# Performance work log

Hardware: AMD Instinct MI355X
Metric: run time of the kernel (lower is better)

The kernel has to match this reference:

```python
import jax, jax.numpy as jnp
import numpy as np

DT = 0.05
TAU = 10.0
V_TH = 2.0
ALPHA = 1.0 - DT / TAU  # membrane leak factor (1 - dt/tau)


def setup_inputs() -> dict:
    key = jax.random.key(0)
    kx, kw = jax.random.split(key)
    B, T, N = 32, 1024, 2048
    x = jax.random.normal(kx, (B, T, N), dtype=jnp.float32)
    # w ~ Normal(0, 1/sqrt(N)) as in torch.nn.init.normal_(std=1/sqrt(N))
    w = jax.random.normal(kw, (N,), dtype=jnp.float32) * float(1.0 / np.sqrt(N))
    return {"x": x, "w": w}


def reference(x, w):
    """LIF recurrence with online eligibility-trace gradient, fused over time.

    Per step t (matching NeuronClass.__call__ then backward_online):
      v   = alpha*v + x_t @ w - v_th * z          (z from previous step, detached)
      z   = 1[v > v_th]
      eps = x_t - v * w                            # [B, N]
      g  += v * eps + (eps @ w) * p                # p is the PRE-update trace
      p   = alpha*p + x_t
    Returns (v_seq [B,T], z_seq [B,T], grad_acc [B,N]).
    """
    B, T, N = x.shape
    alpha = jnp.asarray(ALPHA, x.dtype)
    v_th = jnp.asarray(V_TH, x.dtype)
    xt = jnp.swapaxes(x, 0, 1)  # [T, B, N] for scan over time

    def step(carry, x_t):
        v, z, p, g = carry
        v = alpha * v + x_t @ w - v_th * z          # [B]
        z = (v > v_th).astype(x_t.dtype)            # hard threshold
        eps = x_t - v[:, None] * w                  # [B, N] prediction error
        g = g + v[:, None] * eps + (eps @ w)[:, None] * p
        p = alpha * p + x_t                         # trace updated AFTER use
        return (v, z, p, g), (v, z)

    v0 = jnp.zeros((B,), x.dtype)
    z0 = jnp.zeros((B,), x.dtype)
    p0 = jnp.zeros((B, N), x.dtype)
    g0 = jnp.zeros((B, N), x.dtype)
    (_, _, _, grad_acc), (v_seq, z_seq) = jax.lax.scan(step, (v0, z0, p0, g0), xt)
    return jnp.swapaxes(v_seq, 0, 1), jnp.swapaxes(z_seq, 0, 1), grad_acc
```

## Files before the change

### kernel.cpp

```cpp
#include <hip/hip_runtime.h>


#define ALPHA 0.995f
#define VTH   2.0f

constexpr int B = 32;
constexpr int T = 1024;
constexpr int N = 2048;
constexpr int CT  = 256;
constexpr int NCH = T / CT;
constexpr int TCH = 128;
constexpr int NTC = T / TCH;

typedef float floatx4 __attribute__((ext_vector_type(4)));

__device__ inline floatx4 ntload4(const float* p) {
    return __builtin_nontemporal_load(reinterpret_cast<const floatx4*>(p));
}

__global__ __launch_bounds__(256) void gemv_kernel(const float* __restrict__ x,
                                                   const float* __restrict__ w,
                                                   float* __restrict__ uT) {
    const int wave = threadIdx.x >> 6;
    const int lane = threadIdx.x & 63;
    const int row0 = blockIdx.x * 16 + wave * 4;
    const float* xr = x + (size_t)row0 * N;
    float s0 = 0.f, s1 = 0.f, s2 = 0.f, s3 = 0.f;
#pragma unroll
    for (int k = 0; k < 8; ++k) {
        const int idx = k * 256 + lane * 4;
        const floatx4 wv = *reinterpret_cast<const floatx4*>(w + idx);
        const floatx4 a = ntload4(xr + idx);
        const floatx4 b = ntload4(xr + N + idx);
        const floatx4 c = ntload4(xr + 2 * N + idx);
        const floatx4 d = ntload4(xr + 3 * N + idx);
        s0 += a.x * wv.x + a.y * wv.y + a.z * wv.z + a.w * wv.w;
        s1 += b.x * wv.x + b.y * wv.y + b.z * wv.z + b.w * wv.w;
        s2 += c.x * wv.x + c.y * wv.y + c.z * wv.z + c.w * wv.w;
        s3 += d.x * wv.x + d.y * wv.y + d.z * wv.z + d.w * wv.w;
    }
#pragma unroll
    for (int off = 32; off; off >>= 1) {
        s0 += __shfl_down(s0, off);
        s1 += __shfl_down(s1, off);
        s2 += __shfl_down(s2, off);
        s3 += __shfl_down(s3, off);
    }
    if (lane == 0) {
        const int b0 = row0 >> 10;
        const int t0 = row0 & 1023;
        uT[(t0 + 0) * B + b0] = s0;
        uT[(t0 + 1) * B + b0] = s1;
        uT[(t0 + 2) * B + b0] = s2;
        uT[(t0 + 3) * B + b0] = s3;
    }
}

__global__ __launch_bounds__(256) void scan_kernel(const float* __restrict__ w,
                                                   const float* __restrict__ ubuf,
                                                   float* __restrict__ sbuf,
                                                   float* __restrict__ cbuf,
                                                   float* __restrict__ V2,
                                                   float* __restrict__ out_v,
                                                   float* __restrict__ out_z) {
    __shared__ float u_lds[CT * B];
    __shared__ float v_st[CT * B];
    const int tid  = threadIdx.x;
    const int lane = tid & 63;

    float wacc = 0.f;
#pragma unroll
    for (int i = 0; i < N / 64; ++i) {
        const float wv = w[i * 64 + lane];
        wacc += wv * wv;
    }
#pragma unroll
    for (int off = 32; off; off >>= 1) wacc += __shfl_xor(wacc, off);
    const float wsq = wacc;

    float v = 0.f, z = 0.f, v2 = 0.f;

    for (int cc = 0; cc < NCH; ++cc) {
        const int base = cc * CT * B;
        const int t0   = cc * CT;
#pragma unroll
        for (int k = 0; k < 8; ++k) {
            const int j = k * 1024 + tid * 4;
            *reinterpret_cast<floatx4*>(&u_lds[j]) =
                *reinterpret_cast<const floatx4*>(&ubuf[base + j]);
        }
        __syncthreads();
        if (tid < 32) {
            const int b = tid;
#pragma unroll 4
            for (int tt = 0; tt < CT; ++tt) {
                const float ut = u_lds[tt * 32 + b];
                v = ALPHA * v + ut - VTH * z;
                z = (v > VTH) ? 1.f : 0.f;
                u_lds[tt * 32 + b] = ut - v * wsq;
                v_st[tt * 32 + ((b + tt) & 31)] = v;
                v2 += v * v;
            }
        }
        __syncthreads();
#pragma unroll
        for (int k = 0; k < 8; ++k) {
            const int j = k * 1024 + tid * 4;
            *reinterpret_cast<floatx4*>(&sbuf[base + j]) =
                *reinterpret_cast<const floatx4*>(&u_lds[j]);
        }
#pragma unroll
        for (int k = 0; k < 32; ++k) {
            const int idx = k * 256 + tid;
            const int b  = idx >> 8;
            const int tt = idx & 255;
            const float vv = v_st[tt * 32 + ((b + tt) & 31)];
            out_v[b * T + t0 + tt] = vv;
            out_z[b * T + t0 + tt] = (vv > VTH) ? 1.f : 0.f;
        }
        __syncthreads();
    }
    if (tid < 32) V2[tid] = v2;

    float q = 0.f;
    for (int cc = NCH - 1; cc >= 0; --cc) {
        const int base = cc * CT * B;
        const int t0   = cc * CT;
#pragma unroll
        for (int k = 0; k < 8; ++k) {
            const int j = k * 1024 + tid * 4;
            *reinterpret_cast<floatx4*>(&u_lds[j]) =
                *reinterpret_cast<const floatx4*>(&sbuf[base + j]);
        }
#pragma unroll
        for (int k = 0; k < 32; ++k) {
            const int idx = k * 256 + tid;
            const int b  = idx >> 8;
            const int tt = idx & 255;
            v_st[tt * 32 + ((b + tt) & 31)] = out_v[b * T + t0 + tt];
        }
        __syncthreads();
        if (tid < 32) {
            const int b = tid;
#pragma unroll 4
            for (int tt = CT - 1; tt >= 0; --tt) {
                const float st = u_lds[tt * 32 + b];
                const float vt = v_st[tt * 32 + ((b + tt) & 31)];
                u_lds[tt * 32 + b] = vt + q;
                q = st + ALPHA * q;
            }
        }
        __syncthreads();
#pragma unroll
        for (int k = 0; k < 8; ++k) {
            const int j = k * 1024 + tid * 4;
            *reinterpret_cast<floatx4*>(&cbuf[base + j]) =
                *reinterpret_cast<const floatx4*>(&u_lds[j]);
        }
        __syncthreads();
    }
}

__global__ __launch_bounds__(256) void accum_kernel(const float* __restrict__ x,
                                                    const float* __restrict__ cT,
                                                    float* __restrict__ gpart) {
    __shared__ float cs[TCH];
    const int b   = blockIdx.z;
    const int nc  = blockIdx.y;
    const int tc  = blockIdx.x;
    const int t0  = tc * TCH;
    const int tid = threadIdx.x;
    if (tid < TCH) cs[tid] = cT[(t0 + tid) * B + b];
    __syncthreads();

    const int n = nc * 1024 + tid * 4;
    const float* xb = x + ((size_t)b * T + t0) * N + n;
    floatx4 acc = {0.f, 0.f, 0.f, 0.f};
#pragma unroll 4
    for (int tt = 0; tt < TCH; ++tt) {
        const floatx4 xv = ntload4(xb + (size_t)tt * N);
        const float c = cs[tt];
        acc.x += c * xv.x;
        acc.y += c * xv.y;
        acc.z += c * xv.z;
        acc.w += c * xv.w;
    }
    *reinterpret_cast<floatx4*>(gpart + ((size_t)tc * B + b) * N + n) = acc;
}

__global__ __launch_bounds__(256) void reduce_kernel(const float* __restrict__ gpart,
                                                     const float* __restrict__ w,
                                                     const float* __restrict__ V2,
                                                     float* __restrict__ g) {
    const int i = blockIdx.x * 256 + threadIdx.x;
    const int b = i >> 11;
    const int n = i & (N - 1);
    float acc = -V2[b] * w[n];
#pragma unroll
    for (int tc = 0; tc < NTC; ++tc) acc += gpart[tc * (B * N) + i];
    g[i] = acc;
}

extern "C" void kernel_launch(void* const* d_in, const int* in_sizes, int n_in,
                              void* d_out, int out_size, void* d_ws, size_t ws_size,
                              hipStream_t stream) {
    const float* x = (const float*)d_in[0];
    const float* w = (const float*)d_in[1];

    float* out   = (float*)d_out;
    float* out_v = out;
    float* out_z = out + B * T;
    float* out_g = out + 2 * B * T;

    float* ubuf  = (float*)d_ws;
    float* sbuf  = ubuf + B * T;
    float* cbuf  = sbuf + B * T;
    float* V2    = cbuf + B * T;
    float* gpart = V2 + B;

    gemv_kernel<<<(B * T) / 16, 256, 0, stream>>>(x, w, ubuf);
    scan_kernel<<<1, 256, 0, stream>>>(w, ubuf, sbuf, cbuf, V2, out_v, out_z);
    accum_kernel<<<dim3(NTC, N / 1024, B), 256, 0, stream>>>(x, cbuf, gpart);
    reduce_kernel<<<(B * N) / 256, 256, 0, stream>>>(gpart, w, V2, out_g);
}
```

Measured before the change: 461.9 us.

## Split scan across one block per batch row with batch-major layout

The single-block scan kernel, which handled all 32 batch rows in chunked LDS passes, is replaced by 32 blocks of one wave each. In each block one lane runs the forward and backward recurrences over all timesteps held in LDS, using vectorized register blocks of 32 steps. The gemv output and the c buffer switch from time-major to batch-major layout, which removes the transposed stores and the global sbuf round trip. The accum loop unroll also rises from 4 to 8. The serial chain per row is still done by one lane, but rows now run in parallel on separate CUs and chunk synchronisation is gone.

```diff
diff --git a/kernel.cpp b/kernel.cpp
--- a/kernel.cpp
+++ b/kernel.cpp
@@ -7,8 +7,6 @@
 constexpr int B = 32;
 constexpr int T = 1024;
 constexpr int N = 2048;
-constexpr int CT  = 256;
-constexpr int NCH = T / CT;
 constexpr int TCH = 128;
 constexpr int NTC = T / TCH;
 
@@ -20,7 +18,7 @@
 
 __global__ __launch_bounds__(256) void gemv_kernel(const float* __restrict__ x,
                                                    const float* __restrict__ w,
-                                                   float* __restrict__ uT) {
+                                                   float* __restrict__ u) {
     const int wave = threadIdx.x >> 6;
     const int lane = threadIdx.x & 63;
     const int row0 = blockIdx.x * 16 + wave * 4;
@@ -47,26 +45,23 @@
         s3 += __shfl_down(s3, off);
     }
     if (lane == 0) {
-        const int b0 = row0 >> 10;
-        const int t0 = row0 & 1023;
-        uT[(t0 + 0) * B + b0] = s0;
-        uT[(t0 + 1) * B + b0] = s1;
-        uT[(t0 + 2) * B + b0] = s2;
-        uT[(t0 + 3) * B + b0] = s3;
-    }
-}
-
-__global__ __launch_bounds__(256) void scan_kernel(const float* __restrict__ w,
-                                                   const float* __restrict__ ubuf,
-                                                   float* __restrict__ sbuf,
-                                                   float* __restrict__ cbuf,
-                                                   float* __restrict__ V2,
-                                                   float* __restrict__ out_v,
-                                                   float* __restrict__ out_z) {
-    __shared__ float u_lds[CT * B];
-    __shared__ float v_st[CT * B];
-    const int tid  = threadIdx.x;
-    const int lane = tid & 63;
+        floatx4 r = {s0, s1, s2, s3};
+        *reinterpret_cast<floatx4*>(u + row0) = r;
+    }
+}
+
+__global__ __launch_bounds__(64) void scan_kernel(const float* __restrict__ w,
+                                                  const float* __restrict__ u,
+                                                  float* __restrict__ cbuf,
+                                                  float* __restrict__ V2,
+                                                  float* __restrict__ out_v,
+                                                  float* __restrict__ out_z) {
+    __shared__ float u_lds[T];
+    __shared__ float v_lds[T];
+    __shared__ float s_lds[T];
+    __shared__ float c_lds[T];
+    const int b    = blockIdx.x;
+    const int lane = threadIdx.x;
 
     float wacc = 0.f;
 #pragma unroll
@@ -78,91 +73,84 @@
     for (int off = 32; off; off >>= 1) wacc += __shfl_xor(wacc, off);
     const float wsq = wacc;
 
-    float v = 0.f, z = 0.f, v2 = 0.f;
-
-    for (int cc = 0; cc < NCH; ++cc) {
-        const int base = cc * CT * B;
-        const int t0   = cc * CT;
-#pragma unroll
-        for (int k = 0; k < 8; ++k) {
-            const int j = k * 1024 + tid * 4;
-            *reinterpret_cast<floatx4*>(&u_lds[j]) =
-                *reinterpret_cast<const floatx4*>(&ubuf[base + j]);
+#pragma unroll
+    for (int k = 0; k < T / 256; ++k) {
+        const int j = (k * 64 + lane) * 4;
+        *reinterpret_cast<floatx4*>(&u_lds[j]) =
+            *reinterpret_cast<const floatx4*>(&u[b * T + j]);
+    }
+    __syncthreads();
+
+    if (lane == 0) {
+        float v = 0.f, z = 0.f, v2 = 0.f;
+        for (int cc = 0; cc < T / 32; ++cc) {
+            const int base = cc * 32;
+            floatx4 ub[8];
+#pragma unroll
+            for (int k = 0; k < 8; ++k)
+                ub[k] = *reinterpret_cast<floatx4*>(&u_lds[base + k * 4]);
+            floatx4 vb[8], sb[8];
+#pragma unroll
+            for (int k = 0; k < 8; ++k) {
+#pragma unroll
+                for (int e = 0; e < 4; ++e) {
+                    const float ut = ub[k][e];
+                    v = ALPHA * v + ut - VTH * z;
+                    z = (v > VTH) ? 1.f : 0.f;
+                    vb[k][e] = v;
+                    sb[k][e] = ut - v * wsq;
+                    v2 += v * v;
+                }
+            }
+#pragma unroll
+            for (int k = 0; k < 8; ++k) {
+                *reinterpret_cast<floatx4*>(&v_lds[base + k * 4]) = vb[k];
+                *reinterpret_cast<floatx4*>(&s_lds[base + k * 4]) = sb[k];
+            }
         }
-        __syncthreads();
-        if (tid < 32) {
-            const int b = tid;
-#pragma unroll 4
-            for (int tt = 0; tt < CT; ++tt) {
-                const float ut = u_lds[tt * 32 + b];
-                v = ALPHA * v + ut - VTH * z;
-                z = (v > VTH) ? 1.f : 0.f;
-                u_lds[tt * 32 + b] = ut - v * wsq;
-                v_st[tt * 32 + ((b + tt) & 31)] = v;
-                v2 += v * v;
-            }
+        V2[b] = v2;
+        float q = 0.f;
+        for (int cc = T / 32 - 1; cc >= 0; --cc) {
+            const int base = cc * 32;
+            floatx4 sb[8], vb[8], cb[8];
+#pragma unroll
+            for (int k = 0; k < 8; ++k) {
+                sb[k] = *reinterpret_cast<floatx4*>(&s_lds[base + k * 4]);
+                vb[k] = *reinterpret_cast<floatx4*>(&v_lds[base + k * 4]);
+            }
+#pragma unroll
+            for (int k = 7; k >= 0; --k) {
+#pragma unroll
+                for (int e = 3; e >= 0; --e) {
+                    cb[k][e] = vb[k][e] + q;
+                    q = sb[k][e] + ALPHA * q;
+                }
+            }
+#pragma unroll
+            for (int k = 0; k < 8; ++k)
+                *reinterpret_cast<floatx4*>(&c_lds[base + k * 4]) = cb[k];
         }
-        __syncthreads();
-#pragma unroll
-        for (int k = 0; k < 8; ++k) {
-            const int j = k * 1024 + tid * 4;
-            *reinterpret_cast<floatx4*>(&sbuf[base + j]) =
-                *reinterpret_cast<const floatx4*>(&u_lds[j]);
-        }
-#pragma unroll
-        for (int k = 0; k < 32; ++k) {
-            const int idx = k * 256 + tid;
-            const int b  = idx >> 8;
-            const int tt = idx & 255;
-            const float vv = v_st[tt * 32 + ((b + tt) & 31)];
-            out_v[b * T + t0 + tt] = vv;
-            out_z[b * T + t0 + tt] = (vv > VTH) ? 1.f : 0.f;
-        }
-        __syncthreads();
-    }
-    if (tid < 32) V2[tid] = v2;
-
-    float q = 0.f;
-    for (int cc = NCH - 1; cc >= 0; --cc) {
-        const int base = cc * CT * B;
-        const int t0   = cc * CT;
-#pragma unroll
-        for (int k = 0; k < 8; ++k) {
-            const int j = k * 1024 + tid * 4;
-            *reinterpret_cast<floatx4*>(&u_lds[j]) =
-                *reinterpret_cast<const floatx4*>(&sbuf[base + j]);
-        }
-#pragma unroll
-        for (int k = 0; k < 32; ++k) {
-            const int idx = k * 256 + tid;
-            const int b  = idx >> 8;
-            const int tt = idx & 255;
-            v_st[tt * 32 + ((b + tt) & 31)] = out_v[b * T + t0 + tt];
-        }
-        __syncthreads();
-        if (tid < 32) {
-            const int b = tid;
-#pragma unroll 4
-            for (int tt = CT - 1; tt >= 0; --tt) {
-                const float st = u_lds[tt * 32 + b];
-                const float vt = v_st[tt * 32 + ((b + tt) & 31)];
-                u_lds[tt * 32 + b] = vt + q;
-                q = st + ALPHA * q;
-            }
-        }
-        __syncthreads();
-#pragma unroll
-        for (int k = 0; k < 8; ++k) {
-            const int j = k * 1024 + tid * 4;
-            *reinterpret_cast<floatx4*>(&cbuf[base + j]) =
-                *reinterpret_cast<const floatx4*>(&u_lds[j]);
-        }
-        __syncthreads();
+    }
+    __syncthreads();
+
+#pragma unroll
+    for (int k = 0; k < T / 256; ++k) {
+        const int j = (k * 64 + lane) * 4;
+        const floatx4 vv = *reinterpret_cast<floatx4*>(&v_lds[j]);
+        floatx4 zz;
+        zz.x = (vv.x > VTH) ? 1.f : 0.f;
+        zz.y = (vv.y > VTH) ? 1.f : 0.f;
+        zz.z = (vv.z > VTH) ? 1.f : 0.f;
+        zz.w = (vv.w > VTH) ? 1.f : 0.f;
+        *reinterpret_cast<floatx4*>(&out_v[b * T + j]) = vv;
+        *reinterpret_cast<floatx4*>(&out_z[b * T + j]) = zz;
+        *reinterpret_cast<floatx4*>(&cbuf[b * T + j]) =
+            *reinterpret_cast<floatx4*>(&c_lds[j]);
     }
 }
 
 __global__ __launch_bounds__(256) void accum_kernel(const float* __restrict__ x,
-                                                    const float* __restrict__ cT,
+                                                    const float* __restrict__ c,
                                                     float* __restrict__ gpart) {
     __shared__ float cs[TCH];
     const int b   = blockIdx.z;
@@ -170,20 +158,20 @@
     const int tc  = blockIdx.x;
     const int t0  = tc * TCH;
     const int tid = threadIdx.x;
-    if (tid < TCH) cs[tid] = cT[(t0 + tid) * B + b];
+    if (tid < TCH) cs[tid] = c[b * T + t0 + tid];
     __syncthreads();
 
     const int n = nc * 1024 + tid * 4;
     const float* xb = x + ((size_t)b * T + t0) * N + n;
     floatx4 acc = {0.f, 0.f, 0.f, 0.f};
-#pragma unroll 4
+#pragma unroll 8
     for (int tt = 0; tt < TCH; ++tt) {
         const floatx4 xv = ntload4(xb + (size_t)tt * N);
-        const float c = cs[tt];
-        acc.x += c * xv.x;
-        acc.y += c * xv.y;
-        acc.z += c * xv.z;
-        acc.w += c * xv.w;
+        const float cc = cs[tt];
+        acc.x += cc * xv.x;
+        acc.y += cc * xv.y;
+        acc.z += cc * xv.z;
+        acc.w += cc * xv.w;
     }
     *reinterpret_cast<floatx4*>(gpart + ((size_t)tc * B + b) * N + n) = acc;
 }
@@ -212,14 +200,13 @@
     float* out_z = out + B * T;
     float* out_g = out + 2 * B * T;
 
-    float* ubuf  = (float*)d_ws;
-    float* sbuf  = ubuf + B * T;
-    float* cbuf  = sbuf + B * T;
-    float* V2    = cbuf + B * T;
+    float* u     = (float*)d_ws;
+    float* c     = u + B * T;
+    float* V2    = c + B * T;
     float* gpart = V2 + B;
 
-    gemv_kernel<<<(B * T) / 16, 256, 0, stream>>>(x, w, ubuf);
-    scan_kernel<<<1, 256, 0, stream>>>(w, ubuf, sbuf, cbuf, V2, out_v, out_z);
-    accum_kernel<<<dim3(NTC, N / 1024, B), 256, 0, stream>>>(x, cbuf, gpart);
+    gemv_kernel<<<(B * T) / 16, 256, 0, stream>>>(x, w, u);
+    scan_kernel<<<B, 64, 0, stream>>>(w, u, c, V2, out_v, out_z);
+    accum_kernel<<<dim3(NTC, N / 1024, B), 256, 0, stream>>>(x, c, gpart);
     reduce_kernel<<<(B * N) / 256, 256, 0, stream>>>(gpart, w, V2, out_g);
 }
```

New measurement: 411.4 us. -10.9%, faster.
